# Performance work log

Hardware: AMD Instinct MI355X
Metric: run time of the kernel (lower is better)

## Reference

```python
import jax, jax.numpy as jnp
import numpy as np

B, Nx, Ny = 4, 4096, 8192
M1M, M2M = 8, 8            # modes1, modes2
WID = 32                   # width
HX, HY = 64, 64            # latent grid
DIN, DOUT = 1, 1
S = 16                     # n_subdomains
G = HX * HY
EPS = 1e-6

def _cplx(w):
    return w[..., 0] + 1j * w[..., 1]

def setup_inputs():
    key = jax.random.key(0)
    ks = jax.random.split(key, 20)
    rng = np.random.default_rng(0)
    ind = np.stack([rng.permutation(Ny) for _ in range(B)]).astype(np.int32)
    sep = np.tile(np.arange(S + 1) * (Ny // S), (B, 1)).astype(np.int32)
    d = {}
    d['x'] = jax.random.normal(ks[0], (B, Nx, DIN), jnp.float32)
    d['loc'] = jax.random.uniform(ks[1], (B, Ny, 2), jnp.float32)
    d['ind'] = jnp.asarray(ind)
    d['sep'] = jnp.asarray(sep)
    def lin(k, o, i):
        s = 1.0 / np.sqrt(i)
        return jax.random.uniform(k, (o, i), jnp.float32, -s, s)
    d['W_embed1'] = lin(ks[2], G, Nx); d['b_embed1'] = jnp.zeros((G,), jnp.float32)
    d['W_embed2'] = lin(ks[3], G, Ny); d['b_embed2'] = jnp.zeros((G,), jnp.float32)
    d['W_fc0'] = lin(ks[4], WID, DIN + 2); d['b_fc0'] = jnp.zeros((WID,), jnp.float32)
    sc = 1.0 / (WID * WID)
    d['conv_w1'] = sc * jax.random.uniform(ks[5], (4, WID, WID, M1M, M2M, 2), jnp.float32)
    d['conv_w2'] = sc * jax.random.uniform(ks[6], (4, WID, WID, M1M, M2M, 2), jnp.float32)
    d['wpt'] = jax.random.normal(ks[7], (4, WID, WID), jnp.float32) / np.sqrt(WID)
    d['wpt_b'] = jnp.zeros((4, WID), jnp.float32)
    scn = 1.0 / (WID * S * DOUT)
    d['nu_w1'] = scn * jax.random.uniform(ks[8], (WID, S * DOUT, 2 * M1M + 1, M2M, 2), jnp.float32)
    d['nu_w2'] = scn * jax.random.uniform(ks[9], (WID, S * DOUT, M1M + 1, 1, 2), jnp.float32)
    scw = 1.0 / (S * DOUT)
    d['nu_w'] = scw * jax.random.uniform(ks[10], (S, DOUT), jnp.float32)
    d['nu_b'] = scw * jax.random.uniform(ks[11], (S, DOUT), jnp.float32)
    d['W_de3'] = lin(ks[12], Ny, G); d['b_de3'] = jnp.zeros((Ny,), jnp.float32)
    d['W_fc1'] = lin(ks[13], 128, WID); d['b_fc1'] = jnp.zeros((128,), jnp.float32)
    d['W_fc2'] = lin(ks[14], DOUT, 128); d['b_fc2'] = jnp.zeros((DOUT,), jnp.float32)
    return d

def _spectral_conv(x, w1, w2):
    Bc, C, H, W = x.shape
    xf = jnp.fft.rfft2(x)  # (B,C,H,W//2+1)
    of = jnp.zeros((Bc, w1.shape[1], H, W // 2 + 1), dtype=xf.dtype)
    of = of.at[:, :, :M1M, :M2M].set(jnp.einsum('bixy,ioxy->boxy', xf[:, :, :M1M, :M2M], w1))
    of = of.at[:, :, -M1M:, :M2M].set(jnp.einsum('bixy,ioxy->boxy', xf[:, :, -M1M:, :M2M], w2))
    return jnp.fft.irfft2(of, s=(H, W))

def _nu_spectral_conv(x, loc, ind, sep, nu_w1, nu_w2, nu_w, nu_b):
    Bc, C, H, W = x.shape
    Nyl = loc.shape[1]
    m1, m2 = M1M, M2M
    P1, P2 = 2 * m1 + 1, 2 * m2 + 1
    # centered FFT, padded to odd size (torch: fft2 with s=[H+1-H%2, W+1-W%2], ortho)
    ft = jnp.fft.fftshift(jnp.fft.fft2(x, s=(H + 1 - H % 2, W + 1 - W % 2), norm='ortho'), axes=(-2, -1))
    o1, o2 = ft.shape[-2] // 2, ft.shape[-1] // 2
    im1 = jnp.einsum('bixy,ioxy->boxy', ft[:, :, o1 - m1:o1 + m1 + 1, o2 - m2:o2], nu_w1)  # (B,S*O,P1,m2)
    im2 = jnp.einsum('bixy,ioxy->boxy', ft[:, :, o1 - m1:o1 + 1, o2:o2 + 1], nu_w2)[..., 0]  # (B,S*O,m1+1)
    # hermitian-symmetric image assembly (same fill order as torch code)
    images = jnp.zeros((Bc, S * DOUT, P1, P2), dtype=im1.dtype)
    images = images.at[:, :, :, :m2].set(im1)
    images = images.at[:, :, :, m2 + 1:].set(jnp.flip(im1, (-1, -2)).conj())
    col = jnp.zeros((Bc, S * DOUT, P1), dtype=im1.dtype)
    col = col.at[:, :, m1:].set(jnp.flip(im2, -1).conj())
    col = col.at[:, :, :m1 + 1].set(im2)
    col = col.at[:, :, m1].set(col[:, :, m1].real.astype(im1.dtype))
    images = images.at[:, :, :, m2].set(col).reshape(Bc, S, DOUT, P1, P2)
    # per-point subdomain id: invert (ind, sep) CSR layout
    pos_sub = jax.vmap(lambda s: jnp.searchsorted(s, jnp.arange(Nyl), side='right') - 1)(sep)
    seg = jnp.zeros((Bc, Nyl), jnp.int32).at[jnp.arange(Bc)[:, None], ind].set(pos_sub.astype(jnp.int32))
    ids = (jnp.arange(Bc)[:, None] * S + seg).reshape(-1)
    locf = loc.reshape(Bc * Nyl, 2)
    mn = jax.ops.segment_min(locf, ids, num_segments=Bc * S)[ids]
    mx = jax.ops.segment_max(locf, ids, num_segments=Bc * S)[ids]
    om = (((locf - mn) / (mx - mn + EPS)) * (2 * jnp.pi) - jnp.pi).reshape(Bc, Nyl, 2)
    # exact type-2 NUDFT (torchkbnufft convention: centered grid, ortho norm;
    # module does conj(nufft(conj(images))) => positive-sign exponent)
    n1 = jnp.arange(P1) - m1
    n2 = jnp.arange(P2) - m2
    E = jnp.exp(1j * (om[..., 0, None, None] * n1[:, None] + om[..., 1, None, None] * n2[None, :]))  # (B,Ny,P1,P2)
    vals = jnp.einsum('bsoxy,bpxy->bpso', images, E).real / np.sqrt(P1 * P2)  # (B,Ny,S,O)
    vals = jnp.take_along_axis(vals, seg[:, :, None, None], axis=2)[:, :, 0, :]  # (B,Ny,O)
    out = vals * nu_w[seg] + nu_b[seg]
    return out.transpose(0, 2, 1)  # (B,O,Ny)

def _forward(x, loc, W_embed1, b_embed1, W_embed2, b_embed2, W_fc0, b_fc0,
             conv_w1, conv_w2, wpt, wpt_b, nu_w1, nu_w2, nu_w, nu_b,
             W_de3, b_de3, W_fc1, b_fc1, W_fc2, b_fc2, ind, sep):
    Bc = x.shape[0]
    xe = jnp.einsum('bnd,gn->bgd', x, W_embed1) + b_embed1[None, :, None]
    le = jnp.einsum('bnc,gn->bgc', loc, W_embed2) + b_embed2[None, :, None]
    h = jnp.concatenate([xe, le], axis=-1).reshape(Bc, HX, HY, DIN + 2)
    h = (h @ W_fc0.T + b_fc0).transpose(0, 3, 1, 2)  # (B,width,HX,HY)
    for l in range(4):
        h1 = _spectral_conv(h, _cplx(conv_w1[l]), _cplx(conv_w2[l]))
        h2 = jnp.einsum('oc,bchw->bohw', wpt[l], h) + wpt_b[l][None, :, None, None]
        h = h1 + h2
        if l < 3:
            h = jax.nn.gelu(h, approximate=False)
    x_nu = _nu_spectral_conv(h, loc, ind, sep, _cplx(nu_w1), _cplx(nu_w2), nu_w, nu_b)  # (B,O,Ny)
    hl = h.transpose(0, 2, 3, 1)
    hl = jax.nn.gelu(hl @ W_fc1.T + b_fc1, approximate=False)
    hl = hl @ W_fc2.T + b_fc2                      # (B,HX,HY,O)
    hl = hl.reshape(Bc, G, DOUT).transpose(0, 2, 1)  # (B,O,G)
    hl = hl @ W_de3.T + b_de3                       # (B,O,Ny)
    return (hl + x_nu).transpose(0, 2, 1)           # (B,Ny,O)

def reference(x, loc, ind, sep, W_embed1, b_embed1, W_embed2, b_embed2, W_fc0, b_fc0,
              conv_w1, conv_w2, wpt, wpt_b, nu_w1, nu_w2, nu_w, nu_b,
              W_de3, b_de3, W_fc1, b_fc1, W_fc2, b_fc2):
    return _forward(x, loc, W_embed1, b_embed1, W_embed2, b_embed2, W_fc0, b_fc0,
                    conv_w1, conv_w2, wpt, wpt_b, nu_w1, nu_w2, nu_w, nu_b,
                    W_de3, b_de3, W_fc1, b_fc1, W_fc2, b_fc2, ind, sep)
```

## Files before the change

kernel.cpp:

```cpp
#include <hip/hip_runtime.h>
#include <math.h>

#define BB 4
#define NX 4096
#define NYP 8192
#define GG 4096
#define WIDTH 32
#define SS 16
#define PI_F 3.14159265358979323846f

__device__ __forceinline__ float gelu_exact(float v) {
    return 0.5f * v * (1.0f + erff(v * 0.70710678118654752f));
}

__global__ __launch_bounds__(256, 2) void k_embed(
    const float* __restrict__ x, const float* __restrict__ loc,
    const float* __restrict__ We1, const float* __restrict__ be1,
    const float* __restrict__ We2, const float* __restrict__ be2,
    const float* __restrict__ Wfc0, const float* __restrict__ bfc0,
    float* __restrict__ h0)
{
    int gbase = blockIdx.x * 8;
    int t = threadIdx.x;

    float accx[32];
    #pragma unroll
    for (int k = 0; k < 32; ++k) accx[k] = 0.f;
    for (int n4 = t; n4 < NX / 4; n4 += 256) {
        float4 xb[4];
        #pragma unroll
        for (int b = 0; b < 4; ++b)
            xb[b] = ((const float4*)(x + (size_t)b * NX))[n4];
        float4 w[8];
        #pragma unroll
        for (int r = 0; r < 8; ++r)
            w[r] = ((const float4*)(We1 + (size_t)(gbase + r) * NX))[n4];
        #pragma unroll
        for (int r = 0; r < 8; ++r)
            #pragma unroll
            for (int b = 0; b < 4; ++b)
                accx[r * 4 + b] += w[r].x * xb[b].x + w[r].y * xb[b].y
                                 + w[r].z * xb[b].z + w[r].w * xb[b].w;
    }

    float accl[64];
    #pragma unroll
    for (int k = 0; k < 64; ++k) accl[k] = 0.f;
    for (int n4 = t; n4 < NYP / 4; n4 += 256) {
        float4 p0[4], p1[4];
        #pragma unroll
        for (int b = 0; b < 4; ++b) {
            const float4* lb = (const float4*)(loc + (size_t)b * NYP * 2);
            p0[b] = lb[n4 * 2];
            p1[b] = lb[n4 * 2 + 1];
        }
        float4 w[8];
        #pragma unroll
        for (int r = 0; r < 8; ++r)
            w[r] = ((const float4*)(We2 + (size_t)(gbase + r) * NYP))[n4];
        #pragma unroll
        for (int r = 0; r < 8; ++r)
            #pragma unroll
            for (int b = 0; b < 4; ++b) {
                accl[r * 4 + b]      += w[r].x * p0[b].x + w[r].y * p0[b].z
                                      + w[r].z * p1[b].x + w[r].w * p1[b].z;
                accl[32 + r * 4 + b] += w[r].x * p0[b].y + w[r].y * p0[b].w
                                      + w[r].z * p1[b].y + w[r].w * p1[b].w;
            }
    }

    #pragma unroll
    for (int k = 0; k < 32; ++k)
        for (int off = 32; off > 0; off >>= 1) accx[k] += __shfl_down(accx[k], off);
    #pragma unroll
    for (int k = 0; k < 64; ++k)
        for (int off = 32; off > 0; off >>= 1) accl[k] += __shfl_down(accl[k], off);
    __shared__ float red[4][96];
    __shared__ float tot[96];
    int wave = t >> 6, lane = t & 63;
    if (lane == 0) {
        for (int k = 0; k < 32; ++k) red[wave][k] = accx[k];
        for (int k = 0; k < 64; ++k) red[wave][32 + k] = accl[k];
    }
    __syncthreads();
    if (t < 96) tot[t] = red[0][t] + red[1][t] + red[2][t] + red[3][t];
    __syncthreads();
    if (t < 128) {
        int b = t >> 5, w = t & 31;
        float w0 = Wfc0[w * 3 + 0], w1c = Wfc0[w * 3 + 1], w2c = Wfc0[w * 3 + 2], bb0 = bfc0[w];
        #pragma unroll
        for (int r = 0; r < 8; ++r) {
            int g = gbase + r;
            float xe = tot[r * 4 + b] + be1[g];
            float l0 = tot[32 + r * 4 + b] + be2[g];
            float l1 = tot[64 + r * 4 + b] + be2[g];
            h0[((size_t)(b * WIDTH + w)) * GG + g] = xe * w0 + l0 * w1c + l1 * w2c + bb0;
        }
    }
}

__global__ __launch_bounds__(256) void k_xf(const float* __restrict__ h, float* __restrict__ xf)
{
    int bc = blockIdx.x;
    int t = threadIdx.x;
    __shared__ float sh[64 * 66];
    __shared__ float twc[8 * 64], tws[8 * 64];
    __shared__ float tb64c[64], tb64s[64];
    __shared__ float s1[64 * 8 * 2];
    const float* hp = h + (size_t)bc * 4096;
    for (int i = t; i < 4096; i += 256) sh[(i >> 6) * 66 + (i & 63)] = hp[i];
    for (int i = t; i < 512; i += 256) {
        int ky = i >> 6, y = i & 63;
        float s, c;
        sincosf(-2.f * PI_F * (float)(ky * y) / 64.f, &s, &c);
        twc[i] = c; tws[i] = s;
    }
    if (t < 64) {
        float s, c;
        sincosf(-2.f * PI_F * (float)t / 64.f, &s, &c);
        tb64c[t] = c; tb64s[t] = s;
    }
    __syncthreads();
    for (int task = t; task < 512; task += 256) {
        int xx = task >> 3, ky = task & 7;
        float sr = 0.f, si = 0.f;
        const float* row = sh + xx * 66;
        const float* tc = twc + ky * 64;
        const float* ts = tws + ky * 64;
        for (int y = 0; y < 64; ++y) { sr += row[y] * tc[y]; si += row[y] * ts[y]; }
        s1[(xx * 8 + ky) * 2 + 0] = sr;
        s1[(xx * 8 + ky) * 2 + 1] = si;
    }
    __syncthreads();
    if (t < 128) {
        int kxi = t >> 3, ky = t & 7;
        int kx = (kxi < 8) ? kxi : (kxi - 16);
        float ar = 0.f, ai = 0.f;
        int m = 0;
        for (int xx = 0; xx < 64; ++xx) {
            float c = tb64c[m], s = tb64s[m];
            float vr = s1[(xx * 8 + ky) * 2], vi = s1[(xx * 8 + ky) * 2 + 1];
            ar += vr * c - vi * s;
            ai += vr * s + vi * c;
            m = (m + kx) & 63;
        }
        xf[((size_t)bc * 128 + t) * 2 + 0] = ar;
        xf[((size_t)bc * 128 + t) * 2 + 1] = ai;
    }
}

__global__ __launch_bounds__(256) void k_mix(
    const float* __restrict__ xf,
    const float* __restrict__ w1, const float* __restrict__ w2,
    float* __restrict__ stt)
{
    int blk = blockIdx.x;
    int b = blk >> 5, o = blk & 31;
    int t = threadIdx.x;
    __shared__ float sxf[32 * 128 * 2];
    __shared__ float sof[128 * 2];
    __shared__ float cxc[16 * 64], cxs[16 * 64];
    __shared__ float sw1[32 * 128], sw2[32 * 128];
    const float* xfb = xf + (size_t)b * 32 * 128 * 2;
    for (int i = t; i < 32 * 128 * 2; i += 256) sxf[i] = xfb[i];
    for (int i = t; i < 32 * 128; i += 256) {
        int ii = i >> 7, e = i & 127;
        sw1[i] = w1[((size_t)(ii * 32 + o)) * 128 + e];
        sw2[i] = w2[((size_t)(ii * 32 + o)) * 128 + e];
    }
    for (int i = t; i < 1024; i += 256) {
        int kxi = i >> 6, xx = i & 63;
        int kx = (kxi < 8) ? kxi : (kxi - 16);
        float s, c;
        sincosf(2.f * PI_F * (float)(kx * xx) / 64.f, &s, &c);
        cxc[i] = c; cxs[i] = s;
    }
    __syncthreads();
    if (t < 128) {
        int kxi = t >> 3, ky = t & 7;
        const float* w = (kxi < 8) ? sw1 : sw2;
        int kxw = kxi & 7;
        int e = (kxw * 8 + ky) * 2;
        float ar = 0.f, ai = 0.f;
        #pragma unroll
        for (int i = 0; i < 32; ++i) {
            float wr = w[i * 128 + e], wimag = w[i * 128 + e + 1];
            float xr = sxf[(i * 128 + t) * 2], xi = sxf[(i * 128 + t) * 2 + 1];
            ar += xr * wr - xi * wimag;
            ai += xr * wimag + xi * wr;
        }
        sof[t * 2 + 0] = ar; sof[t * 2 + 1] = ai;
    }
    __syncthreads();
    for (int task = t; task < 512; task += 256) {
        int xx = task >> 3, ky = task & 7;
        float ar = 0.f, ai = 0.f;
        #pragma unroll
        for (int kxi = 0; kxi < 16; ++kxi) {
            float c = cxc[kxi * 64 + xx], s = cxs[kxi * 64 + xx];
            float vr = sof[(kxi * 8 + ky) * 2], vi = sof[(kxi * 8 + ky) * 2 + 1];
            ar += vr * c - vi * s;
            ai += vr * s + vi * c;
        }
        stt[(size_t)blk * 1024 + (xx * 8 + ky) * 2 + 0] = ar * (1.f / 64.f);
        stt[(size_t)blk * 1024 + (xx * 8 + ky) * 2 + 1] = ai * (1.f / 64.f);
    }
}

__global__ __launch_bounds__(256) void k_pw(
    const float* __restrict__ h, const float* __restrict__ stt,
    const float* __restrict__ wpt, const float* __restrict__ wptb,
    float* __restrict__ hout, int do_gelu)
{
    int blk = blockIdx.x;
    int b = blk >> 6, xx = blk & 63;
    int t = threadIdx.x;
    __shared__ float sh[32 * 64];
    __shared__ float sst[32 * 16];
    __shared__ float swp[32 * 32];
    __shared__ float swb[32];
    __shared__ float cy[8 * 64], sy[8 * 64];
    for (int i = t; i < 2048; i += 256) {
        int c = i >> 6, y = i & 63;
        sh[i] = h[((size_t)(b * 32 + c)) * 4096 + xx * 64 + y];
    }
    for (int i = t; i < 512; i += 256) {
        int o = i >> 4, r = i & 15;
        sst[i] = stt[((size_t)(b * 32 + o)) * 1024 + xx * 16 + r];
    }
    for (int i = t; i < 1024; i += 256) swp[i] = wpt[i];
    if (t < 32) swb[t] = wptb[t];
    for (int i = t; i < 512; i += 256) {
        int ky = i >> 6, y = i & 63;
        float s, c;
        sincosf(2.f * PI_F * (float)(ky * y) / 64.f, &s, &c);
        cy[i] = c; sy[i] = s;
    }
    __syncthreads();
    int o = t >> 3, y0 = t & 7;
    float wb = swb[o];
    #pragma unroll
    for (int k = 0; k < 8; ++k) {
        int y = y0 + 8 * k;
        float sp = sst[o * 16 + 0];
        #pragma unroll
        for (int ky = 1; ky < 8; ++ky)
            sp += 2.f * (sst[o * 16 + ky * 2]     * cy[ky * 64 + y]
                       - sst[o * 16 + ky * 2 + 1] * sy[ky * 64 + y]);
        sp *= (1.f / 64.f);
        float pw = wb;
        #pragma unroll
        for (int c = 0; c < 32; ++c)
            pw += swp[o * 32 + c] * sh[c * 64 + y];
        float v = sp + pw;
        if (do_gelu) v = gelu_exact(v);
        hout[((size_t)(b * 32 + o)) * 4096 + xx * 64 + y] = v;
    }
}

__global__ __launch_bounds__(256) void k_nu_fm(const float* __restrict__ h, float* __restrict__ Fm)
{
    int bc = blockIdx.x;
    int t = threadIdx.x;
    __shared__ float sh[64 * 66];
    __shared__ float twc[9 * 64], tws[9 * 64];
    __shared__ float t65c[65], t65s[65];
    __shared__ float s1[64 * 9 * 2];
    const float* hp = h + (size_t)bc * 4096;
    for (int i = t; i < 4096; i += 256) sh[(i >> 6) * 66 + (i & 63)] = hp[i];
    for (int i = t; i < 9 * 64; i += 256) {
        int bbi = i >> 6, y = i & 63;
        float s, c;
        sincosf(-2.f * PI_F * (float)((bbi - 8) * y) / 65.f, &s, &c);
        twc[i] = c; tws[i] = s;
    }
    if (t < 65) {
        float s, c;
        sincosf(-2.f * PI_F * (float)t / 65.f, &s, &c);
        t65c[t] = c; t65s[t] = s;
    }
    __syncthreads();
    for (int task = t; task < 64 * 9; task += 256) {
        int xx = task / 9, bbi = task % 9;
        float sr = 0.f, si = 0.f;
        const float* row = sh + xx * 66;
        const float* tc = twc + bbi * 64;
        const float* ts = tws + bbi * 64;
        for (int y = 0; y < 64; ++y) { sr += row[y] * tc[y]; si += row[y] * ts[y]; }
        s1[(xx * 9 + bbi) * 2 + 0] = sr;
        s1[(xx * 9 + bbi) * 2 + 1] = si;
    }
    __syncthreads();
    for (int task = t; task < 17 * 9; task += 256) {
        int ai2 = task / 9, bbi = task % 9;
        int afreq = ai2 - 8;
        float ar = 0.f, aim = 0.f;
        int m = 0;
        for (int xx = 0; xx < 64; ++xx) {
            float c = t65c[m], s = t65s[m];
            float vr = s1[(xx * 9 + bbi) * 2], vi = s1[(xx * 9 + bbi) * 2 + 1];
            ar += vr * c - vi * s;
            aim += vr * s + vi * c;
            m += afreq;
            if (m < 0) m += 65;
            else if (m >= 65) m -= 65;
        }
        Fm[((size_t)bc * 153 + task) * 2 + 0] = ar * (1.f / 65.f);
        Fm[((size_t)bc * 153 + task) * 2 + 1] = aim * (1.f / 65.f);
    }
}

__global__ __launch_bounds__(256) void k_nu_img(
    const float* __restrict__ Fm, const float* __restrict__ nw1, const float* __restrict__ nw2,
    float* __restrict__ images)
{
    int blk = blockIdx.x;
    int b = blk >> 4, s = blk & 15;
    int t = threadIdx.x;
    __shared__ float im1[17 * 8 * 2];
    __shared__ float im2[9 * 2];
    if (t < 136) {
        int xx = t >> 3, y = t & 7;
        float ar = 0.f, ai = 0.f;
        for (int i = 0; i < 32; ++i) {
            size_t f0 = (((size_t)(b * 32 + i)) * 153 + xx * 9 + y) * 2;
            size_t w0 = (((size_t)(i * 16 + s) * 17 + xx) * 8 + y) * 2;
            float fr = Fm[f0], fi = Fm[f0 + 1];
            float wr = nw1[w0], wi = nw1[w0 + 1];
            ar += fr * wr - fi * wi;
            ai += fr * wi + fi * wr;
        }
        im1[t * 2] = ar; im1[t * 2 + 1] = ai;
    } else if (t < 145) {
        int k = t - 136;
        float ar = 0.f, ai = 0.f;
        for (int i = 0; i < 32; ++i) {
            size_t f0 = (((size_t)(b * 32 + i)) * 153 + k * 9 + 8) * 2;
            size_t w0 = ((size_t)(i * 16 + s) * 9 + k) * 2;
            float fr = Fm[f0], fi = Fm[f0 + 1];
            float wr = nw2[w0], wi = nw2[w0 + 1];
            ar += fr * wr - fi * wi;
            ai += fr * wi + fi * wr;
        }
        im2[k * 2] = ar; im2[k * 2 + 1] = ai;
    }
    __syncthreads();
    for (int task = t; task < 289; task += 256) {
        int xx = task / 17, y = task % 17;
        float vr, vi;
        if (y < 8)      { vr = im1[(xx * 8 + y) * 2];            vi = im1[(xx * 8 + y) * 2 + 1]; }
        else if (y > 8) { int sx = 16 - xx, sy2 = 16 - y;
                          vr = im1[(sx * 8 + sy2) * 2];          vi = -im1[(sx * 8 + sy2) * 2 + 1]; }
        else {
            if (xx < 8)       { vr = im2[xx * 2];        vi = im2[xx * 2 + 1]; }
            else if (xx == 8) { vr = im2[16];            vi = 0.f; }
            else              { vr = im2[(16 - xx) * 2]; vi = -im2[(16 - xx) * 2 + 1]; }
        }
        images[((size_t)blk * 289 + task) * 2 + 0] = vr;
        images[((size_t)blk * 289 + task) * 2 + 1] = vi;
    }
}

__global__ __launch_bounds__(256) void k_nudft(
    const int* __restrict__ ind, const int* __restrict__ sep, const float* __restrict__ loc,
    const float* __restrict__ images,
    const float* __restrict__ nu_w, const float* __restrict__ nu_b,
    float* __restrict__ xnu)
{
    int blk = blockIdx.x;
    int b = blk >> 4, s = blk & 15;
    int t = threadIdx.x;
    __shared__ float img[289 * 2];
    __shared__ float r[4][256];
    for (int i = t; i < 578; i += 256) img[i] = images[(size_t)blk * 578 + i];
    int j0 = sep[b * 17 + s], j1 = sep[b * 17 + s + 1];
    float mn0 = 1e30f, mn1 = 1e30f, mx0 = -1e30f, mx1 = -1e30f;
    for (int j = j0 + t; j < j1; j += 256) {
        int p = ind[b * NYP + j];
        float l0 = loc[((size_t)b * NYP + p) * 2];
        float l1 = loc[((size_t)b * NYP + p) * 2 + 1];
        mn0 = fminf(mn0, l0); mx0 = fmaxf(mx0, l0);
        mn1 = fminf(mn1, l1); mx1 = fmaxf(mx1, l1);
    }
    r[0][t] = mn0; r[1][t] = mn1; r[2][t] = mx0; r[3][t] = mx1;
    __syncthreads();
    for (int st = 128; st > 0; st >>= 1) {
        if (t < st) {
            r[0][t] = fminf(r[0][t], r[0][t + st]);
            r[1][t] = fminf(r[1][t], r[1][t + st]);
            r[2][t] = fmaxf(r[2][t], r[2][t + st]);
            r[3][t] = fmaxf(r[3][t], r[3][t + st]);
        }
        __syncthreads();
    }
    mn0 = r[0][0]; mn1 = r[1][0]; mx0 = r[2][0]; mx1 = r[3][0];
    float nuw = nu_w[s], nub = nu_b[s];
    const float TWO_PI = 6.28318530717958647692f;
    for (int j = j0 + t; j < j1; j += 256) {
        int p = ind[b * NYP + j];
        float l0 = loc[((size_t)b * NYP + p) * 2];
        float l1 = loc[((size_t)b * NYP + p) * 2 + 1];
        float om0 = (l0 - mn0) / (mx0 - mn0 + 1e-6f) * TWO_PI - PI_F;
        float om1 = (l1 - mn1) / (mx1 - mn1 + 1e-6f) * TWO_PI - PI_F;
        float stepxs, stepxc, stepys, stepyc;
        sincosf(om0, &stepxs, &stepxc);
        sincosf(om1, &stepys, &stepyc);
        float ex_i, ex_r, ey0_i, ey0_r;
        sincosf(-8.f * om0, &ex_i, &ex_r);
        sincosf(-8.f * om1, &ey0_i, &ey0_r);
        float tot = 0.f;
        for (int xx = 0; xx < 17; ++xx) {
            float inr = 0.f, ini = 0.f;
            float eyr = ey0_r, eyi = ey0_i;
            const float* row = img + xx * 34;
            #pragma unroll
            for (int y = 0; y < 17; ++y) {
                float ir = row[y * 2], ii = row[y * 2 + 1];
                inr += ir * eyr - ii * eyi;
                ini += ir * eyi + ii * eyr;
                float nr = eyr * stepyc - eyi * stepys;
                eyi = eyr * stepys + eyi * stepyc;
                eyr = nr;
            }
            tot += ex_r * inr - ex_i * ini;
            float nr = ex_r * stepxc - ex_i * stepxs;
            ex_i = ex_r * stepxs + ex_i * stepxc;
            ex_r = nr;
        }
        xnu[(size_t)b * NYP + p] = (tot * (1.f / 17.f)) * nuw + nub;
    }
}

__global__ __launch_bounds__(256) void k_head(
    const float* __restrict__ h, const float* __restrict__ Wfc1, const float* __restrict__ bfc1,
    const float* __restrict__ Wfc2, const float* __restrict__ bfc2, float* __restrict__ q)
{
    __shared__ float w1s[128 * 32];
    __shared__ float b1s[128];
    __shared__ float w2s[128];
    int t = threadIdx.x;
    for (int i = t; i < 4096; i += 256) w1s[i] = Wfc1[i];
    if (t < 128) { b1s[t] = bfc1[t]; w2s[t] = Wfc2[t]; }
    __syncthreads();
    int id = blockIdx.x * 256 + t;
    int b = id >> 12, g = id & 4095;
    float hv[32];
    #pragma unroll
    for (int c = 0; c < 32; ++c) hv[c] = h[((size_t)(b * 32 + c)) * GG + g];
    float acc = bfc2[0];
    for (int j = 0; j < 128; ++j) {
        float z = b1s[j];
        #pragma unroll
        for (int c = 0; c < 32; ++c) z += w1s[j * 32 + c] * hv[c];
        acc += w2s[j] * gelu_exact(z);
    }
    q[id] = acc;
}

__global__ __launch_bounds__(256) void k_de3(
    const float* __restrict__ Wde3, const float* __restrict__ bde3,
    const float* __restrict__ q, const float* __restrict__ xnu, float* __restrict__ out)
{
    int nbase = blockIdx.x * 8;
    int t = threadIdx.x;
    float acc[32];
    #pragma unroll
    for (int k = 0; k < 32; ++k) acc[k] = 0.f;
    for (int g4 = t; g4 < GG / 4; g4 += 256) {
        float4 qb[4];
        #pragma unroll
        for (int b = 0; b < 4; ++b)
            qb[b] = ((const float4*)(q + (size_t)b * GG))[g4];
        float4 w[8];
        #pragma unroll
        for (int r = 0; r < 8; ++r)
            w[r] = ((const float4*)(Wde3 + (size_t)(nbase + r) * GG))[g4];
        #pragma unroll
        for (int r = 0; r < 8; ++r)
            #pragma unroll
            for (int b = 0; b < 4; ++b)
                acc[r * 4 + b] += w[r].x * qb[b].x + w[r].y * qb[b].y
                                + w[r].z * qb[b].z + w[r].w * qb[b].w;
    }
    #pragma unroll
    for (int k = 0; k < 32; ++k)
        for (int off = 32; off > 0; off >>= 1) acc[k] += __shfl_down(acc[k], off);
    __shared__ float red[4][32];
    int wave = t >> 6, lane = t & 63;
    if (lane == 0)
        for (int k = 0; k < 32; ++k) red[wave][k] = acc[k];
    __syncthreads();
    if (t < 32) {
        float v = red[0][t] + red[1][t] + red[2][t] + red[3][t];
        int r = t >> 2, b = t & 3;
        int n = nbase + r;
        out[(size_t)b * NYP + n] = v + bde3[n] + xnu[(size_t)b * NYP + n];
    }
}

extern "C" void kernel_launch(void* const* d_in, const int* in_sizes, int n_in,
                              void* d_out, int out_size, void* d_ws, size_t ws_size,
                              hipStream_t stream) {
    const float* x    = (const float*)d_in[0];
    const float* loc  = (const float*)d_in[1];
    const int*   ind  = (const int*)d_in[2];
    const int*   sep  = (const int*)d_in[3];
    const float* We1  = (const float*)d_in[4];
    const float* be1  = (const float*)d_in[5];
    const float* We2  = (const float*)d_in[6];
    const float* be2  = (const float*)d_in[7];
    const float* Wfc0 = (const float*)d_in[8];
    const float* bfc0 = (const float*)d_in[9];
    const float* cw1  = (const float*)d_in[10];
    const float* cw2  = (const float*)d_in[11];
    const float* wpt  = (const float*)d_in[12];
    const float* wptb = (const float*)d_in[13];
    const float* nw1  = (const float*)d_in[14];
    const float* nw2  = (const float*)d_in[15];
    const float* nuw  = (const float*)d_in[16];
    const float* nub  = (const float*)d_in[17];
    const float* Wde3 = (const float*)d_in[18];
    const float* bde3 = (const float*)d_in[19];
    const float* Wfc1 = (const float*)d_in[20];
    const float* bfc1 = (const float*)d_in[21];
    const float* Wfc2 = (const float*)d_in[22];
    const float* bfc2 = (const float*)d_in[23];
    float* out = (float*)d_out;

    float* ws     = (float*)d_ws;
    float* hA     = ws;
    float* hB     = hA + (size_t)BB * WIDTH * GG;
    float* xfbuf  = hB + (size_t)BB * WIDTH * GG;
    float* Fm     = xfbuf + (size_t)BB * WIDTH * 128 * 2;
    float* images = Fm + (size_t)BB * WIDTH * 153 * 2;
    float* mnmx   = images + (size_t)BB * SS * 289 * 2;
    float* q      = mnmx + 256;
    float* xnu    = q + (size_t)BB * GG;
    float* sttbuf = xnu + (size_t)BB * NYP;

    k_embed<<<GG / 8, 256, 0, stream>>>(x, loc, We1, be1, We2, be2, Wfc0, bfc0, hA);

    const float* hin = hA;
    float* hout = hB;
    for (int l = 0; l < 4; ++l) {
        k_xf<<<BB * WIDTH, 256, 0, stream>>>(hin, xfbuf);
        k_mix<<<BB * WIDTH, 256, 0, stream>>>(xfbuf,
                                              cw1 + (size_t)l * 16384, cw2 + (size_t)l * 16384,
                                              sttbuf);
        k_pw<<<BB * 64, 256, 0, stream>>>(hin, sttbuf, wpt + l * 1024, wptb + l * 32,
                                          hout, (l < 3) ? 1 : 0);
        float* tmp = (float*)hin; hin = hout; hout = tmp;
    }
    k_nu_fm<<<BB * WIDTH, 256, 0, stream>>>(hin, Fm);
    k_nu_img<<<BB * SS, 256, 0, stream>>>(Fm, nw1, nw2, images);
    k_nudft<<<BB * SS, 256, 0, stream>>>(ind, sep, loc, images, nuw, nub, xnu);
    k_head<<<(BB * GG) / 256, 256, 0, stream>>>(hin, Wfc1, bfc1, Wfc2, bfc2, q);
    k_de3<<<NYP / 8, 256, 0, stream>>>(Wde3, bde3, q, xnu, out);
}
```

Before: 571.6 us.

## Split embed kernel and widen parallelism in mix, nudft and head kernels

Splits the fused embedding kernel into separate loc and x projection kernels that exchange an intermediate buffer, lowering per-thread register pressure. It also uses all 256 threads in k_mix's channel contraction by splitting the sum into two halves. The min/max reduction moves from k_nudft into k_nu_img so k_nudft can run with twice as many blocks. k_head splits its hidden dimension across four waves, launching four times more blocks. Together these aim to raise occupancy and grid size in kernels that are latency-bound, at the cost of an extra launch, extra global traffic and shared-memory reductions.

Result: faster. 545.1 us (-4.6%).

```diff
diff --git a/kernel.cpp b/kernel.cpp
--- a/kernel.cpp
+++ b/kernel.cpp
@@ -13,35 +13,13 @@
     return 0.5f * v * (1.0f + erff(v * 0.70710678118654752f));
 }
 
-__global__ __launch_bounds__(256, 2) void k_embed(
-    const float* __restrict__ x, const float* __restrict__ loc,
-    const float* __restrict__ We1, const float* __restrict__ be1,
-    const float* __restrict__ We2, const float* __restrict__ be2,
-    const float* __restrict__ Wfc0, const float* __restrict__ bfc0,
-    float* __restrict__ h0)
+__global__ __launch_bounds__(256, 2) void k_embed_loc(
+    const float* __restrict__ loc,
+    const float* __restrict__ We2,
+    float* __restrict__ embl)
 {
     int gbase = blockIdx.x * 8;
     int t = threadIdx.x;
-
-    float accx[32];
-    #pragma unroll
-    for (int k = 0; k < 32; ++k) accx[k] = 0.f;
-    for (int n4 = t; n4 < NX / 4; n4 += 256) {
-        float4 xb[4];
-        #pragma unroll
-        for (int b = 0; b < 4; ++b)
-            xb[b] = ((const float4*)(x + (size_t)b * NX))[n4];
-        float4 w[8];
-        #pragma unroll
-        for (int r = 0; r < 8; ++r)
-            w[r] = ((const float4*)(We1 + (size_t)(gbase + r) * NX))[n4];
-        #pragma unroll
-        for (int r = 0; r < 8; ++r)
-            #pragma unroll
-            for (int b = 0; b < 4; ++b)
-                accx[r * 4 + b] += w[r].x * xb[b].x + w[r].y * xb[b].y
-                                 + w[r].z * xb[b].z + w[r].w * xb[b].w;
-    }
 
     float accl[64];
     #pragma unroll
@@ -70,20 +48,63 @@
     }
 
     #pragma unroll
+    for (int k = 0; k < 64; ++k)
+        for (int off = 32; off > 0; off >>= 1) accl[k] += __shfl_down(accl[k], off);
+    __shared__ float red[4][64];
+    __shared__ float tot[64];
+    int wave = t >> 6, lane = t & 63;
+    if (lane == 0)
+        for (int k = 0; k < 64; ++k) red[wave][k] = accl[k];
+    __syncthreads();
+    if (t < 64) tot[t] = red[0][t] + red[1][t] + red[2][t] + red[3][t];
+    __syncthreads();
+    if (t < 64) {
+        int ch = t >> 5, rb = t & 31, r = rb >> 2, b = rb & 3;
+        embl[(size_t)(gbase + r) * 8 + ch * 4 + b] = tot[t];
+    }
+}
+
+__global__ __launch_bounds__(256) void k_embed_x(
+    const float* __restrict__ x,
+    const float* __restrict__ We1, const float* __restrict__ be1,
+    const float* __restrict__ be2,
+    const float* __restrict__ Wfc0, const float* __restrict__ bfc0,
+    const float* __restrict__ embl,
+    float* __restrict__ h0)
+{
+    int gbase = blockIdx.x * 8;
+    int t = threadIdx.x;
+
+    float accx[32];
+    #pragma unroll
+    for (int k = 0; k < 32; ++k) accx[k] = 0.f;
+    for (int n4 = t; n4 < NX / 4; n4 += 256) {
+        float4 xb[4];
+        #pragma unroll
+        for (int b = 0; b < 4; ++b)
+            xb[b] = ((const float4*)(x + (size_t)b * NX))[n4];
+        float4 w[8];
+        #pragma unroll
+        for (int r = 0; r < 8; ++r)
+            w[r] = ((const float4*)(We1 + (size_t)(gbase + r) * NX))[n4];
+        #pragma unroll
+        for (int r = 0; r < 8; ++r)
+            #pragma unroll
+            for (int b = 0; b < 4; ++b)
+                accx[r * 4 + b] += w[r].x * xb[b].x + w[r].y * xb[b].y
+                                 + w[r].z * xb[b].z + w[r].w * xb[b].w;
+    }
+
+    #pragma unroll
     for (int k = 0; k < 32; ++k)
         for (int off = 32; off > 0; off >>= 1) accx[k] += __shfl_down(accx[k], off);
-    #pragma unroll
-    for (int k = 0; k < 64; ++k)
-        for (int off = 32; off > 0; off >>= 1) accl[k] += __shfl_down(accl[k], off);
-    __shared__ float red[4][96];
-    __shared__ float tot[96];
+    __shared__ float red[4][32];
+    __shared__ float tot[32];
     int wave = t >> 6, lane = t & 63;
-    if (lane == 0) {
+    if (lane == 0)
         for (int k = 0; k < 32; ++k) red[wave][k] = accx[k];
-        for (int k = 0; k < 64; ++k) red[wave][32 + k] = accl[k];
-    }
-    __syncthreads();
-    if (t < 96) tot[t] = red[0][t] + red[1][t] + red[2][t] + red[3][t];
+    __syncthreads();
+    if (t < 32) tot[t] = red[0][t] + red[1][t] + red[2][t] + red[3][t];
     __syncthreads();
     if (t < 128) {
         int b = t >> 5, w = t & 31;
@@ -92,8 +113,8 @@
         for (int r = 0; r < 8; ++r) {
             int g = gbase + r;
             float xe = tot[r * 4 + b] + be1[g];
-            float l0 = tot[32 + r * 4 + b] + be2[g];
-            float l1 = tot[64 + r * 4 + b] + be2[g];
+            float l0 = embl[(size_t)g * 8 + b]     + be2[g];
+            float l1 = embl[(size_t)g * 8 + 4 + b] + be2[g];
             h0[((size_t)(b * WIDTH + w)) * GG + g] = xe * w0 + l0 * w1c + l1 * w2c + bb0;
         }
     }
@@ -158,7 +179,7 @@
     int b = blk >> 5, o = blk & 31;
     int t = threadIdx.x;
     __shared__ float sxf[32 * 128 * 2];
-    __shared__ float sof[128 * 2];
+    __shared__ float sof2[2][128 * 2];
     __shared__ float cxc[16 * 64], cxs[16 * 64];
     __shared__ float sw1[32 * 128], sw2[32 * 128];
     const float* xfb = xf + (size_t)b * 32 * 128 * 2;
@@ -176,20 +197,23 @@
         cxc[i] = c; cxs[i] = s;
     }
     __syncthreads();
-    if (t < 128) {
-        int kxi = t >> 3, ky = t & 7;
+    {
+        int half = t >> 7, tt = t & 127;
+        int kxi = tt >> 3, ky = tt & 7;
         const float* w = (kxi < 8) ? sw1 : sw2;
         int kxw = kxi & 7;
         int e = (kxw * 8 + ky) * 2;
         float ar = 0.f, ai = 0.f;
-        #pragma unroll
-        for (int i = 0; i < 32; ++i) {
-            float wr = w[i * 128 + e], wimag = w[i * 128 + e + 1];
-            float xr = sxf[(i * 128 + t) * 2], xi = sxf[(i * 128 + t) * 2 + 1];
+        int i0 = half * 16;
+        #pragma unroll
+        for (int i = 0; i < 16; ++i) {
+            int ii = i0 + i;
+            float wr = w[ii * 128 + e], wimag = w[ii * 128 + e + 1];
+            float xr = sxf[(ii * 128 + tt) * 2], xi = sxf[(ii * 128 + tt) * 2 + 1];
             ar += xr * wr - xi * wimag;
             ai += xr * wimag + xi * wr;
         }
-        sof[t * 2 + 0] = ar; sof[t * 2 + 1] = ai;
+        sof2[half][tt * 2 + 0] = ar; sof2[half][tt * 2 + 1] = ai;
     }
     __syncthreads();
     for (int task = t; task < 512; task += 256) {
@@ -198,7 +222,9 @@
         #pragma unroll
         for (int kxi = 0; kxi < 16; ++kxi) {
             float c = cxc[kxi * 64 + xx], s = cxs[kxi * 64 + xx];
-            float vr = sof[(kxi * 8 + ky) * 2], vi = sof[(kxi * 8 + ky) * 2 + 1];
+            int e = (kxi * 8 + ky) * 2;
+            float vr = sof2[0][e]     + sof2[1][e];
+            float vi = sof2[0][e + 1] + sof2[1][e + 1];
             ar += vr * c - vi * s;
             ai += vr * s + vi * c;
         }
@@ -312,13 +338,25 @@
 
 __global__ __launch_bounds__(256) void k_nu_img(
     const float* __restrict__ Fm, const float* __restrict__ nw1, const float* __restrict__ nw2,
-    float* __restrict__ images)
+    const int* __restrict__ ind, const int* __restrict__ sep, const float* __restrict__ loc,
+    float* __restrict__ images, float* __restrict__ mnmx)
 {
     int blk = blockIdx.x;
     int b = blk >> 4, s = blk & 15;
     int t = threadIdx.x;
     __shared__ float im1[17 * 8 * 2];
     __shared__ float im2[9 * 2];
+    __shared__ float r[4][256];
+    int j0 = sep[b * 17 + s], j1 = sep[b * 17 + s + 1];
+    float mn0 = 1e30f, mn1 = 1e30f, mx0 = -1e30f, mx1 = -1e30f;
+    for (int j = j0 + t; j < j1; j += 256) {
+        int p = ind[b * NYP + j];
+        float l0 = loc[((size_t)b * NYP + p) * 2];
+        float l1 = loc[((size_t)b * NYP + p) * 2 + 1];
+        mn0 = fminf(mn0, l0); mx0 = fmaxf(mx0, l0);
+        mn1 = fminf(mn1, l1); mx1 = fmaxf(mx1, l1);
+    }
+    r[0][t] = mn0; r[1][t] = mn1; r[2][t] = mx0; r[3][t] = mx1;
     if (t < 136) {
         int xx = t >> 3, y = t & 7;
         float ar = 0.f, ai = 0.f;
@@ -345,6 +383,19 @@
         im2[k * 2] = ar; im2[k * 2 + 1] = ai;
     }
     __syncthreads();
+    for (int st = 128; st > 0; st >>= 1) {
+        if (t < st) {
+            r[0][t] = fminf(r[0][t], r[0][t + st]);
+            r[1][t] = fminf(r[1][t], r[1][t + st]);
+            r[2][t] = fmaxf(r[2][t], r[2][t + st]);
+            r[3][t] = fmaxf(r[3][t], r[3][t + st]);
+        }
+        __syncthreads();
+    }
+    if (t == 0) {
+        mnmx[blk * 4 + 0] = r[0][0]; mnmx[blk * 4 + 1] = r[1][0];
+        mnmx[blk * 4 + 2] = r[2][0]; mnmx[blk * 4 + 3] = r[3][0];
+    }
     for (int task = t; task < 289; task += 256) {
         int xx = task / 17, y = task % 17;
         float vr, vi;
@@ -363,40 +414,26 @@
 
 __global__ __launch_bounds__(256) void k_nudft(
     const int* __restrict__ ind, const int* __restrict__ sep, const float* __restrict__ loc,
-    const float* __restrict__ images,
+    const float* __restrict__ images, const float* __restrict__ mnmx,
     const float* __restrict__ nu_w, const float* __restrict__ nu_b,
     float* __restrict__ xnu)
 {
     int blk = blockIdx.x;
-    int b = blk >> 4, s = blk & 15;
+    int bs = blk >> 1, half = blk & 1;
+    int b = bs >> 4, s = bs & 15;
     int t = threadIdx.x;
     __shared__ float img[289 * 2];
-    __shared__ float r[4][256];
-    for (int i = t; i < 578; i += 256) img[i] = images[(size_t)blk * 578 + i];
+    for (int i = t; i < 578; i += 256) img[i] = images[(size_t)bs * 578 + i];
+    __syncthreads();
     int j0 = sep[b * 17 + s], j1 = sep[b * 17 + s + 1];
-    float mn0 = 1e30f, mn1 = 1e30f, mx0 = -1e30f, mx1 = -1e30f;
-    for (int j = j0 + t; j < j1; j += 256) {
-        int p = ind[b * NYP + j];
-        float l0 = loc[((size_t)b * NYP + p) * 2];
-        float l1 = loc[((size_t)b * NYP + p) * 2 + 1];
-        mn0 = fminf(mn0, l0); mx0 = fmaxf(mx0, l0);
-        mn1 = fminf(mn1, l1); mx1 = fmaxf(mx1, l1);
-    }
-    r[0][t] = mn0; r[1][t] = mn1; r[2][t] = mx0; r[3][t] = mx1;
-    __syncthreads();
-    for (int st = 128; st > 0; st >>= 1) {
-        if (t < st) {
-            r[0][t] = fminf(r[0][t], r[0][t + st]);
-            r[1][t] = fminf(r[1][t], r[1][t + st]);
-            r[2][t] = fmaxf(r[2][t], r[2][t + st]);
-            r[3][t] = fmaxf(r[3][t], r[3][t + st]);
-        }
-        __syncthreads();
-    }
-    mn0 = r[0][0]; mn1 = r[1][0]; mx0 = r[2][0]; mx1 = r[3][0];
+    int cnt = j1 - j0, per = (cnt + 1) >> 1;
+    int st = j0 + half * per;
+    int en = min(j1, st + per);
+    float mn0 = mnmx[bs * 4], mn1 = mnmx[bs * 4 + 1];
+    float mx0 = mnmx[bs * 4 + 2], mx1 = mnmx[bs * 4 + 3];
     float nuw = nu_w[s], nub = nu_b[s];
     const float TWO_PI = 6.28318530717958647692f;
-    for (int j = j0 + t; j < j1; j += 256) {
+    for (int j = st + t; j < en; j += 256) {
         int p = ind[b * NYP + j];
         float l0 = loc[((size_t)b * NYP + p) * 2];
         float l1 = loc[((size_t)b * NYP + p) * 2 + 1];
@@ -438,23 +475,32 @@
     __shared__ float w1s[128 * 32];
     __shared__ float b1s[128];
     __shared__ float w2s[128];
+    __shared__ float sacc[4][64];
     int t = threadIdx.x;
     for (int i = t; i < 4096; i += 256) w1s[i] = Wfc1[i];
     if (t < 128) { b1s[t] = bfc1[t]; w2s[t] = Wfc2[t]; }
     __syncthreads();
-    int id = blockIdx.x * 256 + t;
+    int pt = t & 63, jq = t >> 6;
+    int id = blockIdx.x * 64 + pt;
     int b = id >> 12, g = id & 4095;
     float hv[32];
     #pragma unroll
     for (int c = 0; c < 32; ++c) hv[c] = h[((size_t)(b * 32 + c)) * GG + g];
-    float acc = bfc2[0];
-    for (int j = 0; j < 128; ++j) {
+    float acc = 0.f;
+    int jbase = jq * 32;
+    for (int jj = 0; jj < 32; ++jj) {
+        int j = jbase + jj;
         float z = b1s[j];
         #pragma unroll
         for (int c = 0; c < 32; ++c) z += w1s[j * 32 + c] * hv[c];
         acc += w2s[j] * gelu_exact(z);
     }
-    q[id] = acc;
+    sacc[jq][pt] = acc;
+    __syncthreads();
+    if (t < 64) {
+        int id2 = blockIdx.x * 64 + t;
+        q[id2] = sacc[0][t] + sacc[1][t] + sacc[2][t] + sacc[3][t] + bfc2[0];
+    }
 }
 
 __global__ __launch_bounds__(256) void k_de3(
@@ -537,8 +583,10 @@
     float* q      = mnmx + 256;
     float* xnu    = q + (size_t)BB * GG;
     float* sttbuf = xnu + (size_t)BB * NYP;
-
-    k_embed<<<GG / 8, 256, 0, stream>>>(x, loc, We1, be1, We2, be2, Wfc0, bfc0, hA);
+    float* embl   = sttbuf + (size_t)BB * WIDTH * 1024;
+
+    k_embed_loc<<<GG / 8, 256, 0, stream>>>(loc, We2, embl);
+    k_embed_x<<<GG / 8, 256, 0, stream>>>(x, We1, be1, be2, Wfc0, bfc0, embl, hA);
 
     const float* hin = hA;
     float* hout = hB;
@@ -552,8 +600,8 @@
         float* tmp = (float*)hin; hin = hout; hout = tmp;
     }
     k_nu_fm<<<BB * WIDTH, 256, 0, stream>>>(hin, Fm);
-    k_nu_img<<<BB * SS, 256, 0, stream>>>(Fm, nw1, nw2, images);
-    k_nudft<<<BB * SS, 256, 0, stream>>>(ind, sep, loc, images, nuw, nub, xnu);
-    k_head<<<(BB * GG) / 256, 256, 0, stream>>>(hin, Wfc1, bfc1, Wfc2, bfc2, q);
+    k_nu_img<<<BB * SS, 256, 0, stream>>>(Fm, nw1, nw2, ind, sep, loc, images, mnmx);
+    k_nudft<<<BB * SS * 2, 256, 0, stream>>>(ind, sep, loc, images, mnmx, nuw, nub, xnu);
+    k_head<<<(BB * GG) / 64, 256, 0, stream>>>(hin, Wfc1, bfc1, Wfc2, bfc2, q);
     k_de3<<<NYP / 8, 256, 0, stream>>>(Wde3, bde3, q, xnu, out);
 }
```
